# Kernel optimization log

Measured on AMD Instinct MI355X. Metric: run time of the kernel, lower is better.

Reference implementation:

```python
import jax, jax.numpy as jnp
import numpy as np

B, N, K = 32, 64, 128          # batch, atoms per cell, channel width (128x0e + 128x1o)
R_MAX = 5.0
NUM_BESSEL = 8
P_CUT = 5                       # num_polynomial_cutoff
AVG_NEIGH = 16.0                # avg_num_neighbors
H_MLP = 512                     # hidden_dimensions_size, n_hidden_dimensions = 2
FEAT = 5 * K                    # ((num_interactions-1)*4 + 1) * 128 = 640


def silu(x):
    return x * jax.nn.sigmoid(x)


def _bessel_cutoff(r, mask):
    # Bessel radial basis * polynomial cutoff (MACE), masked on valid edges.
    n = jnp.arange(1, NUM_BESSEL + 1, dtype=r.dtype)
    rb = jnp.sqrt(2.0 / R_MAX) * jnp.sin(n * (jnp.pi / R_MAX) * r[..., None]) / r[..., None]
    u = r / R_MAX
    p = float(P_CUT)
    fc = 1.0 - 0.5 * (p + 1) * (p + 2) * u**P_CUT + p * (p + 2) * u**(P_CUT + 1) - 0.5 * p * (p + 1) * u**(P_CUT + 2)
    fc = fc * (u < 1.0)
    return rb * (fc * mask)[..., None]


def _sph(uvec):
    # Real spherical harmonics l=0,1,2 (component normalization), uvec: unit edge vectors.
    x, y, z = uvec[..., 0], uvec[..., 1], uvec[..., 2]
    s3, s5, s15 = 3.0**0.5, 5.0**0.5, 15.0**0.5
    Y0 = jnp.ones_like(x)[..., None]
    Y1 = jnp.stack([s3 * x, s3 * y, s3 * z], -1)
    Y2 = jnp.stack([s15 * x * y, s15 * y * z, 0.5 * s5 * (3 * z * z - 1.0),
                    s15 * x * z, 0.5 * s15 * (x * x - y * y)], -1)
    return Y0, Y1, Y2


def _radial_mlp(x, w0, b0, w1, b1, w2, b2, w3, b3):
    h = silu(x @ w0 + b0)
    h = silu(h @ w1 + b1)
    h = silu(h @ w2 + b2)
    return h @ w3 + b3


def setup_inputs() -> dict:
    key = jax.random.key(0)
    ks = jax.random.split(key, 32)
    f32 = jnp.float32

    def lin(k, fan_in, shape):
        return (jax.random.normal(k, shape, dtype=f32) / np.sqrt(fan_in)).astype(f32)

    inp = {
        "noisy_relative_positions": jax.random.uniform(ks[0], (B, N, 3), dtype=f32),
        "time": jax.random.uniform(ks[1], (B, 1), dtype=f32),
        "unit_cell": (11.0 * jnp.eye(3, dtype=f32) + 0.3 * jax.random.uniform(ks[2], (B, 3, 3), dtype=f32)),
        "w_embed": lin(ks[3], 1, (K,)),
        # interaction 1 radial MLP: 8 -> 64 -> 64 -> 64 -> 3*K (weights for l=0,1,2 paths)
        "r1_w0": lin(ks[4], NUM_BESSEL, (NUM_BESSEL, 64)), "r1_b0": jnp.zeros((64,), f32),
        "r1_w1": lin(ks[5], 64, (64, 64)), "r1_b1": jnp.zeros((64,), f32),
        "r1_w2": lin(ks[6], 64, (64, 64)), "r1_b2": jnp.zeros((64,), f32),
        "r1_w3": lin(ks[7], 64, (64, 3 * K)), "r1_b3": jnp.zeros((3 * K,), f32),
        "mix1_l0": lin(ks[8], K, (K, K)),
        "mix1_l1": lin(ks[9], K, (K, K)),
        "mix1_l2": lin(ks[10], K, (K, K)),
        # interaction 2 radial MLP: 8 -> 64 -> 64 -> 64 -> 2*K (paths 0e x 0e -> 0e, 1o x 1o -> 0e)
        "r2_w0": lin(ks[11], NUM_BESSEL, (NUM_BESSEL, 64)), "r2_b0": jnp.zeros((64,), f32),
        "r2_w1": lin(ks[12], 64, (64, 64)), "r2_b1": jnp.zeros((64,), f32),
        "r2_w2": lin(ks[13], 64, (64, 64)), "r2_b2": jnp.zeros((64,), f32),
        "r2_w3": lin(ks[14], 64, (64, 2 * K)), "r2_b3": jnp.zeros((2 * K,), f32),
        "mix2": lin(ks[15], K, (K, K)),
        # readout MLP: 641 -> 512 -> 512 -> 3
        "mlp_w0": lin(ks[16], FEAT + 1, (FEAT + 1, H_MLP)), "mlp_b0": jnp.zeros((H_MLP,), f32),
        "mlp_w1": lin(ks[17], H_MLP, (H_MLP, H_MLP)), "mlp_b1": jnp.zeros((H_MLP,), f32),
        "mlp_w2": lin(ks[18], H_MLP, (H_MLP, 3)), "mlp_b2": jnp.zeros((3,), f32),
    }
    return inp


def reference(noisy_relative_positions, time, unit_cell, w_embed,
              r1_w0, r1_b0, r1_w1, r1_b1, r1_w2, r1_b2, r1_w3, r1_b3,
              mix1_l0, mix1_l1, mix1_l2,
              r2_w0, r2_b0, r2_w1, r2_b1, r2_w2, r2_b2, r2_w3, r2_b3, mix2,
              mlp_w0, mlp_b0, mlp_w1, mlp_b1, mlp_w2, mlp_b2):
    frac = noisy_relative_positions                      # [B,N,3] fractional
    d = frac[:, :, None, :] - frac[:, None, :, :]        # [B,N,N,3]
    d = d - jnp.round(d)                                 # minimum-image PBC
    dc = jnp.einsum('bijc,bcd->bijd', d, unit_cell)      # cartesian displacements
    r = jnp.sqrt(jnp.maximum(jnp.sum(dc * dc, -1), 1e-12))
    mask = (r < R_MAX) & (~jnp.eye(N, dtype=bool))[None]
    r_safe = jnp.where(mask, r, 1.0)
    uvec = dc / r_safe[..., None] * mask[..., None]      # unit edge vectors (0 off-edge)

    rad = _bessel_cutoff(r_safe, mask)                   # [B,N,N,8]
    Y0, Y1, Y2 = _sph(uvec)                              # [B,N,N,1|3|5]

    h0 = jnp.broadcast_to(w_embed, (B, N, K))            # element embedding (single species)

    # ---- interaction 1: radial-weighted tensor product h_j (x) Y_l, scatter over j ----
    we = _radial_mlp(rad, r1_w0, r1_b0, r1_w1, r1_b1, r1_w2, r1_b2, r1_w3, r1_b3)
    we = we.reshape(B, N, N, 3, K) * mask[..., None, None]
    hj = h0[:, None, :, :]                               # sender features [B,1,N,K]
    msg0 = jnp.einsum('bijk,bijm->bimk', we[..., 0, :] * hj, Y0)[:, :, 0] / AVG_NEIGH  # [B,N,K]
    msg1 = jnp.einsum('bijk,bijm->bimk', we[..., 1, :] * hj, Y1) / AVG_NEIGH           # [B,N,3,K]
    msg2 = jnp.einsum('bijk,bijm->bimk', we[..., 2, :] * hj, Y2) / AVG_NEIGH           # [B,N,5,K]

    s1 = msg0 @ mix1_l0 + jnp.sum(msg2 * msg2, axis=2) @ mix1_l2   # scalars [B,N,K]
    v1 = jnp.einsum('bimk,kc->bimc', msg1, mix1_l1)                # vectors [B,N,3,K]
    h1 = silu(s1)

    # ---- interaction 2: scalar output from 0e x 0e and 1o x 1o -> 0e paths ----
    we2 = _radial_mlp(rad, r2_w0, r2_b0, r2_w1, r2_b1, r2_w2, r2_b2, r2_w3, r2_b3)
    we2 = we2.reshape(B, N, N, 2, K) * mask[..., None, None]
    msg_a = jnp.sum(we2[..., 0, :] * h1[:, None, :, :], axis=2)    # [B,N,K]
    inv = jnp.einsum('bijm,bjmk->bijk', Y1, v1)                    # Y1 . v1_j invariant
    msg_b = jnp.sum(we2[..., 1, :] * inv, axis=2)
    s2 = ((msg_a + msg_b) / AVG_NEIGH) @ mix2                      # [B,N,K]

    # node_feats: layer1 full irreps (128x0e + 128x1o -> 512) + layer2 scalars (128) = 640
    node_feats = jnp.concatenate([s1, v1.reshape(B, N, 3 * K), s2], axis=-1)

    t = jnp.broadcast_to(time[:, None, :], (B, N, 1))
    x = jnp.concatenate([node_feats, t], axis=-1)                  # [B,N,641]
    x = jax.nn.relu(x @ mlp_w0 + mlp_b0)
    x = jax.nn.relu(x @ mlp_w1 + mlp_b1)
    return x @ mlp_w2 + mlp_b2                                     # [B,N,3]
```

## Files before the change

### kernel.cpp

```cpp
#include <hip/hip_runtime.h>
#include <math.h>

#define B_ 32
#define N_ 64
#define K_ 128
#define NPAIR (B_*N_*N_)
#define PREP_TOTAL 733184

typedef __attribute__((ext_vector_type(8))) short short8;
typedef __attribute__((ext_vector_type(8))) __bf16 bf16x8;
typedef __attribute__((ext_vector_type(4))) float floatx4;

__device__ __forceinline__ float silu_f(float x) {
    return x / (1.0f + expf(-x));
}

__device__ __forceinline__ short f2bf(float x) {
    union { float f; unsigned u; } v; v.f = x;
    unsigned r = (v.u + 0x7FFFu + ((v.u >> 16) & 1u)) >> 16;
    return (short)r;
}
__device__ __forceinline__ float bf2f(short s) {
    union { unsigned u; float f; } v;
    v.u = ((unsigned)(unsigned short)s) << 16;
    return v.f;
}
__device__ __forceinline__ bf16x8 ld_frag(const short* p) {
    short8 r = *(const short8*)p;
    return __builtin_bit_cast(bf16x8, r);
}

__global__ __launch_bounds__(256) void prep_kernel(
    const float* __restrict__ r1w1, const float* __restrict__ r1w2,
    const float* __restrict__ r2w1, const float* __restrict__ r2w2,
    const float* __restrict__ r2w3, const float* __restrict__ mw0,
    const float* __restrict__ mw1,
    const float* __restrict__ r1w0, const float* __restrict__ r2w0,
    const float* __restrict__ r1w3,
    const float* __restrict__ l0, const float* __restrict__ l1,
    const float* __restrict__ l2,
    short* __restrict__ dst)
{
    int idx = blockIdx.x * 256 + threadIdx.x;
    if (idx >= PREP_TOTAL) return;
    short v;
    if (idx < 4096) {
        int h = idx >> 6, k = idx & 63; v = f2bf(r1w1[k*64 + h]);
    } else if (idx < 8192) {
        int i = idx - 4096; int h = i >> 6, k = i & 63; v = f2bf(r1w2[k*64 + h]);
    } else if (idx < 12288) {
        int i = idx - 8192; int h = i >> 6, k = i & 63; v = f2bf(r2w1[k*64 + h]);
    } else if (idx < 16384) {
        int i = idx - 12288; int h = i >> 6, k = i & 63; v = f2bf(r2w2[k*64 + h]);
    } else if (idx < 32768) {
        int i = idx - 16384; int col = i >> 6, h = i & 63; v = f2bf(r2w3[h*256 + col]);
    } else if (idx < 393216) {
        int i = idx - 32768; int n = i / 704, k = i - n*704;
        v = (k < 641) ? f2bf(mw0[(size_t)k*512 + n]) : (short)0;
    } else if (idx < 655360) {
        int i = idx - 393216; int n = i >> 9, k = i & 511;
        v = f2bf(mw1[(size_t)k*512 + n]);
    } else if (idx < 657408) {
        int i = idx - 655360; int h = i >> 5, k = i & 31;
        v = (k < 8) ? f2bf(r1w0[k*64 + h]) : (short)0;
    } else if (idx < 659456) {
        int i = idx - 657408; int h = i >> 5, k = i & 31;
        v = (k < 8) ? f2bf(r2w0[k*64 + h]) : (short)0;
    } else if (idx < 684032) {
        int i = idx - 659456; int col = i >> 6, h = i & 63;
        v = f2bf(r1w3[(size_t)h*384 + col]);
    } else {
        int i = idx - 684032; int n = i >> 7, k = i & 127;
        float src = (n < 128) ? l0[(size_t)k*128 + n]
                  : (n < 256) ? l1[(size_t)k*128 + (n-128)]
                              : l2[(size_t)k*128 + (n-256)];
        v = f2bf(src);
    }
    dst[idx] = v;
}

__device__ __forceinline__ void mfma_layer(
    const short* __restrict__ src, const short* __restrict__ WT,
    const float* __restrict__ bias, short* __restrict__ dst,
    int wv, int qd, int nn)
{
    floatx4 acc[4];
    #pragma unroll
    for (int tt = 0; tt < 4; tt++) acc[tt] = (floatx4){0.f, 0.f, 0.f, 0.f};
    #pragma unroll
    for (int ks = 0; ks < 64; ks += 32) {
        bf16x8 a = ld_frag(&src[(wv*16 + nn)*72 + ks + qd*8]);
        #pragma unroll
        for (int tt = 0; tt < 4; tt++) {
            bf16x8 b = ld_frag(&WT[(tt*16 + nn)*64 + ks + qd*8]);
            acc[tt] = __builtin_amdgcn_mfma_f32_16x16x32_bf16(a, b, acc[tt], 0, 0, 0);
        }
    }
    #pragma unroll
    for (int tt = 0; tt < 4; tt++) {
        int col = tt*16 + nn;
        float bv = bias[col];
        #pragma unroll
        for (int i = 0; i < 4; i++) {
            int row = wv*16 + qd*4 + i;
            dst[row*72 + col] = f2bf(silu_f(acc[tt][i] + bv));
        }
    }
}

__device__ __forceinline__ void mfma_layer_T(
    const short* __restrict__ src, const short* __restrict__ WT,
    const float* __restrict__ bias, short* __restrict__ dstT,
    int wv, int qd, int nn)
{
    floatx4 acc[4];
    #pragma unroll
    for (int tt = 0; tt < 4; tt++) acc[tt] = (floatx4){0.f, 0.f, 0.f, 0.f};
    #pragma unroll
    for (int ks = 0; ks < 64; ks += 32) {
        bf16x8 a = ld_frag(&src[(wv*16 + nn)*72 + ks + qd*8]);
        #pragma unroll
        for (int tt = 0; tt < 4; tt++) {
            bf16x8 b = ld_frag(&WT[(tt*16 + nn)*64 + ks + qd*8]);
            acc[tt] = __builtin_amdgcn_mfma_f32_16x16x32_bf16(a, b, acc[tt], 0, 0, 0);
        }
    }
    #pragma unroll
    for (int tt = 0; tt < 4; tt++) {
        int col = tt*16 + nn;
        float bv = bias[col];
        #pragma unroll
        for (int i = 0; i < 4; i++) {
            int row = wv*16 + qd*4 + i;
            dstT[col*72 + row] = f2bf(silu_f(acc[tt][i] + bv));
        }
    }
}

__device__ __forceinline__ void mfma_layer_gout(
    const short* __restrict__ src, const short* __restrict__ WT,
    const float* __restrict__ bias, short* __restrict__ gdst,
    int wv, int qd, int nn)
{
    floatx4 acc[4];
    #pragma unroll
    for (int tt = 0; tt < 4; tt++) acc[tt] = (floatx4){0.f, 0.f, 0.f, 0.f};
    #pragma unroll
    for (int ks = 0; ks < 64; ks += 32) {
        bf16x8 a = ld_frag(&src[(wv*16 + nn)*72 + ks + qd*8]);
        #pragma unroll
        for (int tt = 0; tt < 4; tt++) {
            bf16x8 b = ld_frag(&WT[(tt*16 + nn)*64 + ks + qd*8]);
            acc[tt] = __builtin_amdgcn_mfma_f32_16x16x32_bf16(a, b, acc[tt], 0, 0, 0);
        }
    }
    #pragma unroll
    for (int tt = 0; tt < 4; tt++) {
        int col = tt*16 + nn;
        float bv = bias[col];
        #pragma unroll
        for (int i = 0; i < 4; i++) {
            int row = wv*16 + qd*4 + i;
            gdst[row*64 + col] = f2bf(silu_f(acc[tt][i] + bv));
        }
    }
}

__device__ __forceinline__ void mfma_layer0(
    const short* __restrict__ rad_bf, const short* __restrict__ w0T,
    const float* __restrict__ b0, short* __restrict__ dst,
    int wv, int qd, int nn)
{
    floatx4 acc[4];
    #pragma unroll
    for (int tt = 0; tt < 4; tt++) acc[tt] = (floatx4){0.f, 0.f, 0.f, 0.f};
    bf16x8 a = ld_frag(&rad_bf[(wv*16 + nn)*32 + qd*8]);
    #pragma unroll
    for (int tt = 0; tt < 4; tt++) {
        bf16x8 b = ld_frag(&w0T[(tt*16 + nn)*32 + qd*8]);
        acc[tt] = __builtin_amdgcn_mfma_f32_16x16x32_bf16(a, b, acc[tt], 0, 0, 0);
    }
    #pragma unroll
    for (int tt = 0; tt < 4; tt++) {
        int col = tt*16 + nn;
        float bv = b0[col];
        #pragma unroll
        for (int i = 0; i < 4; i++) {
            int row = wv*16 + qd*4 + i;
            dst[row*72 + col] = f2bf(silu_f(acc[tt][i] + bv));
        }
    }
}

__global__ __launch_bounds__(256) void pass1x_kernel(
    const float* __restrict__ pos, const float* __restrict__ cell,
    const float* __restrict__ wemb,
    const short* __restrict__ w0T1, const float* __restrict__ b01,
    const short* __restrict__ w1T1, const float* __restrict__ b11,
    const short* __restrict__ w2T1, const float* __restrict__ b21,
    const short* __restrict__ w3T1, const float* __restrict__ b31,
    const short* __restrict__ w0T2, const float* __restrict__ b02,
    const short* __restrict__ w1T2, const float* __restrict__ b12,
    const short* __restrict__ w2T2, const float* __restrict__ b22,
    const short* __restrict__ lcatT, const float* __restrict__ timeg,
    float* __restrict__ geo4, short* __restrict__ hc2,
    float* __restrict__ h1g, float* __restrict__ v1g, short* __restrict__ featsb)
{
    __shared__ __align__(16) char smem[41472];
    short* actA   = (short*)smem;
    short* actB   = (short*)(smem + 9216);
    short* actC   = (short*)(smem + 18432);
    short* actD   = (short*)(smem + 27648);
    float* msg    = (float*)(smem + 9216);
    float* q_s    = (float*)(smem + 9216 + 4608);
    short* rad_bf = (short*)(smem + 36864);
    short* Ym_bf  = (short*)(smem + 36864);
    short* G_bf   = (short*)(smem + 36864 + 2304);
    short* A2     = (short*)smem;
    float* Psa    = (float*)(smem + 9216);
    float* Psb    = Psa + 128;

    int t = threadIdx.x;
    int wv = t >> 6, lane = t & 63, qd = lane >> 4, nn = lane & 15;
    int node = blockIdx.x;
    int b = node >> 6;
    int irow = node & 63;
    size_t pbase = (size_t)node * 64;

    float vals[9];
    float sy9[9];
    if (t < 64) {
        int j = t;
        const float* pi = pos + (size_t)(b*N_ + irow)*3;
        const float* pj = pos + (size_t)(b*N_ + j)*3;
        float d0 = pi[0]-pj[0], d1 = pi[1]-pj[1], d2 = pi[2]-pj[2];
        d0 -= rintf(d0); d1 -= rintf(d1); d2 -= rintf(d2);
        const float* C = cell + b*9;
        float dc0 = d0*C[0] + d1*C[3] + d2*C[6];
        float dc1 = d0*C[1] + d1*C[4] + d2*C[7];
        float dc2 = d0*C[2] + d1*C[5] + d2*C[8];
        float r2 = fmaxf(dc0*dc0 + dc1*dc1 + dc2*dc2, 1e-12f);
        float r = sqrtf(r2);
        bool m = (r < 5.0f) && (irow != j);
        float mf = m ? 1.0f : 0.0f;
        float rs = m ? r : 1.0f;
        float inv_rs = 1.0f / rs;
        float x = dc0*inv_rs*mf, y = dc1*inv_rs*mf, z = dc2*inv_rs*mf;
        float u = r * 0.2f;
        float u2 = u*u, u4 = u2*u2, u5 = u4*u;
        float fc = 1.0f - 21.0f*u5 + 35.0f*u5*u - 15.0f*u5*u2;
        fc = (u < 1.0f) ? fc : 0.0f;
        float pref = 0.6324555320336759f * inv_rs * (fc * mf);
        float w = 0.6283185307179586f * rs;
        float sw = sinf(w), cw = cosf(w);
        float twoc = 2.0f * cw;
        float sm = 0.0f, s = sw;
        #pragma unroll
        for (int n = 0; n < 8; n++) {
            rad_bf[j*32 + n] = f2bf(pref * s);
            float nx = twoc*s - sm;
            sm = s; s = nx;
        }
        #pragma unroll
        for (int k = 8; k < 32; k++) rad_bf[j*32 + k] = 0;
        const float s3  = 1.7320508075688772f;
        const float s5  = 2.23606797749979f;
        const float s15 = 3.872983346207417f;
        vals[0] = mf;
        vals[1] = s3*x; vals[2] = s3*y; vals[3] = s3*z;
        vals[4] = s15*x*y;
        vals[5] = s15*y*z;
        vals[6] = 0.5f*s5*(3.0f*z*z - 1.0f);
        vals[7] = s15*x*z;
        vals[8] = 0.5f*s15*(x*x - y*y);
        *(float4*)&geo4[(pbase + j)*4] = make_float4(mf, vals[1], vals[2], vals[3]);
        #pragma unroll
        for (int m9 = 0; m9 < 9; m9++) {
            float sv = vals[m9];
            #pragma unroll
            for (int off = 32; off > 0; off >>= 1) sv += __shfl_xor(sv, off);
            sy9[m9] = sv;
        }
    }
    __syncthreads();

    mfma_layer0(rad_bf, w0T1, b01, actA, wv, qd, nn);
    mfma_layer0(rad_bf, w0T2, b02, actC, wv, qd, nn);
    __syncthreads();

    if (t < 64) {
        int j = t;
        #pragma unroll
        for (int m9 = 0; m9 < 9; m9++) Ym_bf[m9*72 + j] = f2bf(vals[m9]);
        #pragma unroll
        for (int m9 = 9; m9 < 16; m9++) Ym_bf[m9*72 + j] = 0;
        #pragma unroll
        for (int m9 = 0; m9 < 9; m9++)
            if (j == m9) *(float*)(&Ym_bf[m9*72 + 64]) = sy9[m9];
    }
    mfma_layer(actA, w1T1, b11, actB, wv, qd, nn);
    mfma_layer(actC, w1T2, b12, actD, wv, qd, nn);
    __syncthreads();

    mfma_layer_T(actB, w2T1, b21, actA, wv, qd, nn);
    mfma_layer_gout(actD, w2T2, b22, hc2 + (size_t)node*4096, wv, qd, nn);
    __syncthreads();

    {
        floatx4 acc = (floatx4){0.f, 0.f, 0.f, 0.f};
        #pragma unroll
        for (int ks = 0; ks < 64; ks += 32) {
            bf16x8 a = ld_frag(&Ym_bf[nn*72 + ks + qd*8]);
            bf16x8 bb = ld_frag(&actA[(wv*16 + nn)*72 + ks + qd*8]);
            acc = __builtin_amdgcn_mfma_f32_16x16x32_bf16(a, bb, acc, 0, 0, 0);
        }
        #pragma unroll
        for (int i = 0; i < 4; i++)
            G_bf[(qd*4 + i)*72 + wv*16 + nn] = f2bf(acc[i]);
    }
    __syncthreads();

    {
        floatx4 acc[6];
        #pragma unroll
        for (int tt = 0; tt < 6; tt++) acc[tt] = (floatx4){0.f, 0.f, 0.f, 0.f};
        #pragma unroll
        for (int ks = 0; ks < 64; ks += 32) {
            bf16x8 a = ld_frag(&G_bf[nn*72 + ks + qd*8]);
            #pragma unroll
            for (int tt = 0; tt < 6; tt++) {
                bf16x8 bb = ld_frag(&w3T1[((wv*6 + tt)*16 + nn)*64 + ks + qd*8]);
                acc[tt] = __builtin_amdgcn_mfma_f32_16x16x32_bf16(a, bb, acc[tt], 0, 0, 0);
            }
        }
        #pragma unroll
        for (int tt = 0; tt < 6; tt++) {
            int col = (wv*6 + tt)*16 + nn;
            #pragma unroll
            for (int i = 0; i < 4; i++) {
                int m9 = qd*4 + i;
                if (m9 < 9) {
                    int c = (m9 == 0) ? 0 : ((m9 < 4) ? 1 : 2);
                    int k = col - c*128;
                    if (k >= 0 && k < 128) {
                        float sym = *(const float*)(&Ym_bf[m9*72 + 64]);
                        msg[m9*128 + k] = (acc[tt][i] + sym*b31[col]) * wemb[k] * 0.0625f;
                    }
                }
            }
        }
    }
    __syncthreads();

    if (t < 128) {
        int k = t;
        float acc = 0.f;
        #pragma unroll
        for (int m9 = 4; m9 < 9; m9++) { float v = msg[m9*128 + k]; acc += v*v; }
        q_s[k] = acc;
    }
    __syncthreads();

    for (int idx = t; idx < 2048; idx += 256) {
        int r = idx >> 7, k = idx & 127;
        float v = (r == 0) ? msg[k]
                : (r == 1) ? q_s[k]
                : (r < 5)  ? msg[(r-1)*128 + k] : 0.f;
        A2[r*136 + k] = f2bf(v);
    }
    __syncthreads();

    {
        bf16x8 pa[4];
        #pragma unroll
        for (int ksI = 0; ksI < 4; ksI++)
            pa[ksI] = ld_frag(&A2[nn*136 + ksI*32 + qd*8]);
        floatx4 acc[6];
        #pragma unroll
        for (int tt = 0; tt < 6; tt++) acc[tt] = (floatx4){0.f, 0.f, 0.f, 0.f};
        #pragma unroll
        for (int tt = 0; tt < 6; tt++) {
            int tn = wv*6 + tt;
            #pragma unroll
            for (int ksI = 0; ksI < 4; ksI++) {
                bf16x8 bf = ld_frag(&lcatT[((size_t)(tn*16 + nn))*128 + ksI*32 + qd*8]);
                acc[tt] = __builtin_amdgcn_mfma_f32_16x16x32_bf16(pa[ksI], bf, acc[tt], 0, 0, 0);
            }
        }
        #pragma unroll
        for (int tt = 0; tt < 6; tt++) {
            int n = (wv*6 + tt)*16 + nn;
            #pragma unroll
            for (int i = 0; i < 4; i++) {
                int r = qd*4 + i;
                float val = acc[tt][i];
                if (r == 0 && n < 128) Psa[n] = val;
                else if (r == 1 && n >= 256) Psb[n - 256] = val;
                else if (r >= 2 && r < 5 && n >= 128 && n < 256) {
                    int m9 = r - 2, cc = n - 128;
                    v1g[(size_t)node*384 + m9*128 + cc] = val;
                    featsb[(size_t)node*704 + 128 + m9*128 + cc] = f2bf(val);
                }
            }
        }
    }
    __syncthreads();

    if (t < 128) {
        float s1 = Psa[t] + Psb[t];
        featsb[(size_t)node*704 + t] = f2bf(s1);
        h1g[(size_t)node*128 + t] = silu_f(s1);
    } else if (t == 128) {
        featsb[(size_t)node*704 + 640] = f2bf(timeg[b]);
    } else if (t > 128 && t < 192) {
        featsb[(size_t)node*704 + 640 + (t - 128)] = 0;
    }
}

__global__ __launch_bounds__(256) void pass2b_kernel(
    const float* __restrict__ geo4,
    const short* __restrict__ hc2,
    const short* __restrict__ w3T, const float* __restrict__ b3,
    const float* __restrict__ mix2,
    const float* __restrict__ h1g, const float* __restrict__ v1g,
    short* __restrict__ featsb)
{
    __shared__ float mask_s[64];
    __shared__ float Y1s[64*4];
    __shared__ float msgab[128];
    int t = threadIdx.x;
    int wv = t >> 6, lane = t & 63, qd = lane >> 4, nn = lane & 15;
    int node = blockIdx.x;
    int b = node >> 6;
    size_t pbase = (size_t)node * 64;

    if (t < 64) {
        float4 g = *(const float4*)&geo4[(pbase + t)*4];
        mask_s[t] = g.x;
        Y1s[t*4 + 0] = g.y; Y1s[t*4 + 1] = g.z; Y1s[t*4 + 2] = g.w;
    }
    if (t >= 64 && t < 192) msgab[t - 64] = 0.f;
    __syncthreads();

    const short* hcb = hc2 + (size_t)node*4096;
    bf16x8 a0 = ld_frag(&hcb[(wv*16 + nn)*64 + qd*8]);
    bf16x8 a1 = ld_frag(&hcb[(wv*16 + nn)*64 + 32 + qd*8]);
    for (int g = 0; g < 4; g++) {
        floatx4 acc[4];
        #pragma unroll
        for (int tt = 0; tt < 4; tt++) acc[tt] = (floatx4){0.f, 0.f, 0.f, 0.f};
        #pragma unroll
        for (int tt = 0; tt < 4; tt++) {
            int ct = g*4 + tt;
            bf16x8 b0f = ld_frag(&w3T[(ct*16 + nn)*64 + qd*8]);
            bf16x8 b1f = ld_frag(&w3T[(ct*16 + nn)*64 + 32 + qd*8]);
            acc[tt] = __builtin_amdgcn_mfma_f32_16x16x32_bf16(a0, b0f, acc[tt], 0, 0, 0);
            acc[tt] = __builtin_amdgcn_mfma_f32_16x16x32_bf16(a1, b1f, acc[tt], 0, 0, 0);
        }
        #pragma unroll
        for (int tt = 0; tt < 4; tt++) {
            int col = (g*4 + tt)*16 + nn;
            float bias = b3[col];
            int k = col & 127;
            float p = 0.f;
            if (col < 128) {
                #pragma unroll
                for (int i = 0; i < 4; i++) {
                    int j = wv*16 + qd*4 + i;
                    float we = (acc[tt][i] + bias) * mask_s[j];
                    p += we * h1g[((size_t)b*64 + j)*128 + k];
                }
            } else {
                #pragma unroll
                for (int i = 0; i < 4; i++) {
                    int j = wv*16 + qd*4 + i;
                    float we = (acc[tt][i] + bias) * mask_s[j];
                    const float* vb = &v1g[((size_t)b*64 + j)*384 + k];
                    float inv = Y1s[j*4+0]*vb[0] + Y1s[j*4+1]*vb[128] + Y1s[j*4+2]*vb[256];
                    p += we * inv;
                }
            }
            p += __shfl_xor(p, 16);
            p += __shfl_xor(p, 32);
            if (qd == 0) atomicAdd(&msgab[k], p);
        }
    }
    __syncthreads();

    if (t < 128) {
        int c = t;
        float acc = 0.f;
        for (int k = 0; k < 128; k++) acc += msgab[k] * mix2[k*128 + c];
        featsb[(size_t)node*704 + 512 + c] = f2bf(acc * 0.0625f);
    }
}

__global__ __launch_bounds__(256) void gemm_mfma_kernel(
    const short* __restrict__ A, int lda,
    const short* __restrict__ BT, int ldb, int K,
    const float* __restrict__ bias, short* __restrict__ Cout, int ldo)
{
    __shared__ short As[64*72];
    __shared__ short Bs[64*72];
    int t = threadIdx.x;
    int wv = t >> 6, lane = t & 63, qd = lane >> 4, nn = lane & 15;
    int m0 = blockIdx.x * 64, n0 = blockIdx.y * 64;
    floatx4 acc[4];
    #pragma unroll
    for (int tt = 0; tt < 4; tt++) acc[tt] = (floatx4){0.f, 0.f, 0.f, 0.f};

    for (int kc = 0; kc < K; kc += 64) {
        for (int s = t; s < 512; s += 256) {
            int j = s >> 3, kk = (s & 7) * 8;
            *(uint4*)&As[j*72 + kk] = *(const uint4*)&A[(size_t)(m0 + j)*lda + kc + kk];
            *(uint4*)&Bs[j*72 + kk] = *(const uint4*)&BT[(size_t)(n0 + j)*ldb + kc + kk];
        }
        __syncthreads();
        #pragma unroll
        for (int ks = 0; ks < 64; ks += 32) {
            bf16x8 a = ld_frag(&As[(wv*16 + nn)*72 + ks + qd*8]);
            #pragma unroll
            for (int tt = 0; tt < 4; tt++) {
                bf16x8 bb = ld_frag(&Bs[(tt*16 + nn)*72 + ks + qd*8]);
                acc[tt] = __builtin_amdgcn_mfma_f32_16x16x32_bf16(a, bb, acc[tt], 0, 0, 0);
            }
        }
        __syncthreads();
    }
    #pragma unroll
    for (int tt = 0; tt < 4; tt++) {
        int n = n0 + tt*16 + nn;
        float bv = bias[n];
        #pragma unroll
        for (int i = 0; i < 4; i++) {
            int m = m0 + wv*16 + qd*4 + i;
            Cout[(size_t)m*ldo + n] = f2bf(fmaxf(acc[tt][i] + bv, 0.f));
        }
    }
}

__global__ __launch_bounds__(64) void final3_kernel(
    const short* __restrict__ H, const float* __restrict__ w2,
    const float* __restrict__ b2, float* __restrict__ out)
{
    int node = blockIdx.x, lane = threadIdx.x;
    float a0 = 0.f, a1 = 0.f, a2 = 0.f;
    #pragma unroll
    for (int r = 0; r < 8; r++) {
        int k = r*64 + lane;
        float h = bf2f(H[(size_t)node*512 + k]);
        a0 += h * w2[k*3 + 0];
        a1 += h * w2[k*3 + 1];
        a2 += h * w2[k*3 + 2];
    }
    #pragma unroll
    for (int off = 32; off > 0; off >>= 1) {
        a0 += __shfl_down(a0, off);
        a1 += __shfl_down(a1, off);
        a2 += __shfl_down(a2, off);
    }
    if (lane == 0) {
        out[(size_t)node*3 + 0] = a0 + b2[0];
        out[(size_t)node*3 + 1] = a1 + b2[1];
        out[(size_t)node*3 + 2] = a2 + b2[2];
    }
}

extern "C" void kernel_launch(void* const* d_in, const int* in_sizes, int n_in,
                              void* d_out, int out_size, void* d_ws, size_t ws_size,
                              hipStream_t stream) {
    const float* pos   = (const float*)d_in[0];
    const float* timeg = (const float*)d_in[1];
    const float* cell  = (const float*)d_in[2];
    const float* wemb  = (const float*)d_in[3];
    const float* r1w0  = (const float*)d_in[4];
    const float* r1b0  = (const float*)d_in[5];
    const float* r1w1  = (const float*)d_in[6];
    const float* r1b1  = (const float*)d_in[7];
    const float* r1w2  = (const float*)d_in[8];
    const float* r1b2  = (const float*)d_in[9];
    const float* r1w3  = (const float*)d_in[10];
    const float* r1b3  = (const float*)d_in[11];
    const float* l0    = (const float*)d_in[12];
    const float* l1    = (const float*)d_in[13];
    const float* l2    = (const float*)d_in[14];
    const float* r2w0  = (const float*)d_in[15];
    const float* r2b0  = (const float*)d_in[16];
    const float* r2w1  = (const float*)d_in[17];
    const float* r2b1  = (const float*)d_in[18];
    const float* r2w2  = (const float*)d_in[19];
    const float* r2b2  = (const float*)d_in[20];
    const float* r2w3  = (const float*)d_in[21];
    const float* r2b3  = (const float*)d_in[22];
    const float* mix2  = (const float*)d_in[23];
    const float* mw0   = (const float*)d_in[24];
    const float* mb0   = (const float*)d_in[25];
    const float* mw1   = (const float*)d_in[26];
    const float* mb1   = (const float*)d_in[27];
    const float* mw2   = (const float*)d_in[28];
    const float* mb2   = (const float*)d_in[29];

    float* ws    = (float*)d_ws;
    float* geo4  = ws;
    float* h1    = geo4 + (size_t)NPAIR*4;
    float* v1    = h1   + (size_t)B_*N_*K_;
    short* featsb = (short*)(v1 + (size_t)B_*N_*3*K_);
    short* prep  = featsb + (size_t)2048*704;
    short* w1T_1 = prep;
    short* w2T_1 = prep + 4096;
    short* w1T_2 = prep + 8192;
    short* w2T_2 = prep + 12288;
    short* w3T_2 = prep + 16384;
    short* wT0   = prep + 32768;
    short* wT1   = prep + 393216;
    short* w0T_1 = prep + 655360;
    short* w0T_2 = prep + 657408;
    short* w3T_1 = prep + 659456;
    short* lcatT = prep + 684032;
    short* hc2   = prep + PREP_TOTAL;
    short* h0bb  = hc2 + (size_t)2048*4096;
    short* h1bb  = h0bb + (size_t)2048*512;

    prep_kernel<<<(PREP_TOTAL + 255)/256, 256, 0, stream>>>(
        r1w1, r1w2, r2w1, r2w2, r2w3, mw0, mw1,
        r1w0, r2w0, r1w3, l0, l1, l2, prep);
    pass1x_kernel<<<B_*N_, 256, 0, stream>>>(pos, cell, wemb,
        w0T_1, r1b0, w1T_1, r1b1, w2T_1, r1b2, w3T_1, r1b3,
        w0T_2, r2b0, w1T_2, r2b1, w2T_2, r2b2,
        lcatT, timeg, geo4, hc2, h1, v1, featsb);
    pass2b_kernel<<<B_*N_, 256, 0, stream>>>(geo4, hc2,
        w3T_2, r2b3, mix2, h1, v1, featsb);
    dim3 g0(32, 8);
    gemm_mfma_kernel<<<g0, 256, 0, stream>>>(featsb, 704, wT0, 704, 704, mb0, h0bb, 512);
    gemm_mfma_kernel<<<g0, 256, 0, stream>>>(h0bb, 512, wT1, 512, 512, mb1, h1bb, 512);
    final3_kernel<<<B_*N_, 64, 0, stream>>>(h1bb, mw2, mb2, (float*)d_out);
}
```

Measured before the change: 288.5 us.

## Split pass1 into MLP kernel and back-projection kernel to cut LDS footprint

```diff
diff --git a/kernel.cpp b/kernel.cpp
--- a/kernel.cpp
+++ b/kernel.cpp
@@ -12,7 +12,7 @@
 typedef __attribute__((ext_vector_type(4))) float floatx4;
 
 __device__ __forceinline__ float silu_f(float x) {
-    return x / (1.0f + expf(-x));
+    return x / (1.0f + __expf(-x));
 }
 
 __device__ __forceinline__ short f2bf(float x) {
@@ -192,34 +192,20 @@
     }
 }
 
-__global__ __launch_bounds__(256) void pass1x_kernel(
+__global__ __launch_bounds__(256) void mlpx_kernel(
     const float* __restrict__ pos, const float* __restrict__ cell,
-    const float* __restrict__ wemb,
     const short* __restrict__ w0T1, const float* __restrict__ b01,
     const short* __restrict__ w1T1, const float* __restrict__ b11,
     const short* __restrict__ w2T1, const float* __restrict__ b21,
-    const short* __restrict__ w3T1, const float* __restrict__ b31,
     const short* __restrict__ w0T2, const float* __restrict__ b02,
     const short* __restrict__ w1T2, const float* __restrict__ b12,
     const short* __restrict__ w2T2, const float* __restrict__ b22,
-    const short* __restrict__ lcatT, const float* __restrict__ timeg,
-    float* __restrict__ geo4, short* __restrict__ hc2,
-    float* __restrict__ h1g, float* __restrict__ v1g, short* __restrict__ featsb)
-{
-    __shared__ __align__(16) char smem[41472];
-    short* actA   = (short*)smem;
-    short* actB   = (short*)(smem + 9216);
-    short* actC   = (short*)(smem + 18432);
-    short* actD   = (short*)(smem + 27648);
-    float* msg    = (float*)(smem + 9216);
-    float* q_s    = (float*)(smem + 9216 + 4608);
-    short* rad_bf = (short*)(smem + 36864);
-    short* Ym_bf  = (short*)(smem + 36864);
-    short* G_bf   = (short*)(smem + 36864 + 2304);
-    short* A2     = (short*)smem;
-    float* Psa    = (float*)(smem + 9216);
-    float* Psb    = Psa + 128;
-
+    float* __restrict__ geo4, short* __restrict__ hc2, short* __restrict__ Gg)
+{
+    __shared__ __align__(16) short actA[64*72];
+    __shared__ __align__(16) short actB[64*72];
+    __shared__ __align__(16) short rad_bf[64*32];
+    __shared__ __align__(16) short Ym_bf[16*72];
     int t = threadIdx.x;
     int wv = t >> 6, lane = t & 63, qd = lane >> 4, nn = lane & 15;
     int node = blockIdx.x;
@@ -227,8 +213,6 @@
     int irow = node & 63;
     size_t pbase = (size_t)node * 64;
 
-    float vals[9];
-    float sy9[9];
     if (t < 64) {
         int j = t;
         const float* pi = pos + (size_t)(b*N_ + irow)*3;
@@ -266,6 +250,7 @@
         const float s3  = 1.7320508075688772f;
         const float s5  = 2.23606797749979f;
         const float s15 = 3.872983346207417f;
+        float vals[9];
         vals[0] = mf;
         vals[1] = s3*x; vals[2] = s3*y; vals[3] = s3*z;
         vals[4] = s15*x*y;
@@ -275,35 +260,34 @@
         vals[8] = 0.5f*s15*(x*x - y*y);
         *(float4*)&geo4[(pbase + j)*4] = make_float4(mf, vals[1], vals[2], vals[3]);
         #pragma unroll
+        for (int m9 = 0; m9 < 9; m9++) Ym_bf[m9*72 + j] = f2bf(vals[m9]);
+        #pragma unroll
+        for (int m9 = 9; m9 < 16; m9++) Ym_bf[m9*72 + j] = 0;
+        #pragma unroll
         for (int m9 = 0; m9 < 9; m9++) {
             float sv = vals[m9];
             #pragma unroll
             for (int off = 32; off > 0; off >>= 1) sv += __shfl_xor(sv, off);
-            sy9[m9] = sv;
-        }
-    }
-    __syncthreads();
-
+            if (j == m9)
+                *(float*)(Gg + (size_t)node*1152 + m9*72 + 64) = sv;
+        }
+    }
+    __syncthreads();
+
+    mfma_layer0(rad_bf, w0T2, b02, actA, wv, qd, nn);
+    __syncthreads();
+
+    mfma_layer(actA, w1T2, b12, actB, wv, qd, nn);
+    __syncthreads();
+
+    mfma_layer_gout(actB, w2T2, b22, hc2 + (size_t)node*4096, wv, qd, nn);
     mfma_layer0(rad_bf, w0T1, b01, actA, wv, qd, nn);
-    mfma_layer0(rad_bf, w0T2, b02, actC, wv, qd, nn);
-    __syncthreads();
-
-    if (t < 64) {
-        int j = t;
-        #pragma unroll
-        for (int m9 = 0; m9 < 9; m9++) Ym_bf[m9*72 + j] = f2bf(vals[m9]);
-        #pragma unroll
-        for (int m9 = 9; m9 < 16; m9++) Ym_bf[m9*72 + j] = 0;
-        #pragma unroll
-        for (int m9 = 0; m9 < 9; m9++)
-            if (j == m9) *(float*)(&Ym_bf[m9*72 + 64]) = sy9[m9];
-    }
+    __syncthreads();
+
     mfma_layer(actA, w1T1, b11, actB, wv, qd, nn);
-    mfma_layer(actC, w1T2, b12, actD, wv, qd, nn);
     __syncthreads();
 
     mfma_layer_T(actB, w2T1, b21, actA, wv, qd, nn);
-    mfma_layer_gout(actD, w2T2, b22, hc2 + (size_t)node*4096, wv, qd, nn);
     __syncthreads();
 
     {
@@ -316,22 +300,45 @@
         }
         #pragma unroll
         for (int i = 0; i < 4; i++)
-            G_bf[(qd*4 + i)*72 + wv*16 + nn] = f2bf(acc[i]);
-    }
+            Gg[(size_t)node*1152 + (qd*4 + i)*72 + wv*16 + nn] = f2bf(acc[i]);
+    }
+}
+
+__global__ __launch_bounds__(256) void back1_kernel(
+    const float* __restrict__ wemb,
+    const short* __restrict__ Gg,
+    const short* __restrict__ w3T, const float* __restrict__ b3,
+    const short* __restrict__ lcatT, const float* __restrict__ timeg,
+    float* __restrict__ h1g, float* __restrict__ v1g, short* __restrict__ featsb)
+{
+    __shared__ __align__(16) short G_lds[16*72];
+    __shared__ __align__(16) short A2[16*136];
+    __shared__ float q_s[128];
+    __shared__ float Ps[256];
+    int t = threadIdx.x;
+    int wv = t >> 6, lane = t & 63, qd = lane >> 4, nn = lane & 15;
+    int node = blockIdx.x;
+    int b = node >> 6;
+
+    if (t < 144)
+        ((uint4*)G_lds)[t] = ((const uint4*)(Gg + (size_t)node*1152))[t];
+    if (t < 128) q_s[t] = 0.f;
+    for (int z = 680 + t; z < 2176; z += 256) A2[z] = 0;
     __syncthreads();
 
     {
+        bf16x8 ga0 = ld_frag(&G_lds[nn*72 + qd*8]);
+        bf16x8 ga1 = ld_frag(&G_lds[nn*72 + 32 + qd*8]);
         floatx4 acc[6];
         #pragma unroll
         for (int tt = 0; tt < 6; tt++) acc[tt] = (floatx4){0.f, 0.f, 0.f, 0.f};
         #pragma unroll
-        for (int ks = 0; ks < 64; ks += 32) {
-            bf16x8 a = ld_frag(&G_bf[nn*72 + ks + qd*8]);
-            #pragma unroll
-            for (int tt = 0; tt < 6; tt++) {
-                bf16x8 bb = ld_frag(&w3T1[((wv*6 + tt)*16 + nn)*64 + ks + qd*8]);
-                acc[tt] = __builtin_amdgcn_mfma_f32_16x16x32_bf16(a, bb, acc[tt], 0, 0, 0);
-            }
+        for (int tt = 0; tt < 6; tt++) {
+            int tn = wv*6 + tt;
+            bf16x8 b0f = ld_frag(&w3T[(tn*16 + nn)*64 + qd*8]);
+            bf16x8 b1f = ld_frag(&w3T[(tn*16 + nn)*64 + 32 + qd*8]);
+            acc[tt] = __builtin_amdgcn_mfma_f32_16x16x32_bf16(ga0, b0f, acc[tt], 0, 0, 0);
+            acc[tt] = __builtin_amdgcn_mfma_f32_16x16x32_bf16(ga1, b1f, acc[tt], 0, 0, 0);
         }
         #pragma unroll
         for (int tt = 0; tt < 6; tt++) {
@@ -343,8 +350,11 @@
                     int c = (m9 == 0) ? 0 : ((m9 < 4) ? 1 : 2);
                     int k = col - c*128;
                     if (k >= 0 && k < 128) {
-                        float sym = *(const float*)(&Ym_bf[m9*72 + 64]);
-                        msg[m9*128 + k] = (acc[tt][i] + sym*b31[col]) * wemb[k] * 0.0625f;
+                        float sym = *(const float*)(&G_lds[m9*72 + 64]);
+                        float val = (acc[tt][i] + sym*b3[col]) * wemb[k] * 0.0625f;
+                        if (m9 == 0)      A2[k] = f2bf(val);
+                        else if (m9 < 4)  A2[(m9+1)*136 + k] = f2bf(val);
+                        else              atomicAdd(&q_s[k], val*val);
                     }
                 }
             }
@@ -352,22 +362,7 @@
     }
     __syncthreads();
 
-    if (t < 128) {
-        int k = t;
-        float acc = 0.f;
-        #pragma unroll
-        for (int m9 = 4; m9 < 9; m9++) { float v = msg[m9*128 + k]; acc += v*v; }
-        q_s[k] = acc;
-    }
-    __syncthreads();
-
-    for (int idx = t; idx < 2048; idx += 256) {
-        int r = idx >> 7, k = idx & 127;
-        float v = (r == 0) ? msg[k]
-                : (r == 1) ? q_s[k]
-                : (r < 5)  ? msg[(r-1)*128 + k] : 0.f;
-        A2[r*136 + k] = f2bf(v);
-    }
+    if (t < 128) A2[136 + t] = f2bf(q_s[t]);
     __syncthreads();
 
     {
@@ -394,8 +389,8 @@
             for (int i = 0; i < 4; i++) {
                 int r = qd*4 + i;
                 float val = acc[tt][i];
-                if (r == 0 && n < 128) Psa[n] = val;
-                else if (r == 1 && n >= 256) Psb[n - 256] = val;
+                if (r == 0 && n < 128) Ps[n] = val;
+                else if (r == 1 && n >= 256) Ps[128 + n - 256] = val;
                 else if (r >= 2 && r < 5 && n >= 128 && n < 256) {
                     int m9 = r - 2, cc = n - 128;
                     v1g[(size_t)node*384 + m9*128 + cc] = val;
@@ -407,7 +402,7 @@
     __syncthreads();
 
     if (t < 128) {
-        float s1 = Psa[t] + Psb[t];
+        float s1 = Ps[t] + Ps[128 + t];
         featsb[(size_t)node*704 + t] = f2bf(s1);
         h1g[(size_t)node*128 + t] = silu_f(s1);
     } else if (t == 128) {
@@ -618,16 +613,19 @@
     short* w3T_1 = prep + 659456;
     short* lcatT = prep + 684032;
     short* hc2   = prep + PREP_TOTAL;
-    short* h0bb  = hc2 + (size_t)2048*4096;
-    short* h1bb  = h0bb + (size_t)2048*512;
+    short* Gg    = hc2 + (size_t)2048*4096;
+    short* h0bb  = hc2;
+    short* h1bb  = hc2 + (size_t)2048*512;
 
     prep_kernel<<<(PREP_TOTAL + 255)/256, 256, 0, stream>>>(
         r1w1, r1w2, r2w1, r2w2, r2w3, mw0, mw1,
         r1w0, r2w0, r1w3, l0, l1, l2, prep);
-    pass1x_kernel<<<B_*N_, 256, 0, stream>>>(pos, cell, wemb,
-        w0T_1, r1b0, w1T_1, r1b1, w2T_1, r1b2, w3T_1, r1b3,
+    mlpx_kernel<<<B_*N_, 256, 0, stream>>>(pos, cell,
+        w0T_1, r1b0, w1T_1, r1b1, w2T_1, r1b2,
         w0T_2, r2b0, w1T_2, r2b1, w2T_2, r2b2,
-        lcatT, timeg, geo4, hc2, h1, v1, featsb);
+        geo4, hc2, Gg);
+    back1_kernel<<<B_*N_, 256, 0, stream>>>(wemb, Gg,
+        w3T_1, r1b3, lcatT, timeg, h1, v1, featsb);
     pass2b_kernel<<<B_*N_, 256, 0, stream>>>(geo4, hc2,
         w3T_2, r2b3, mix2, h1, v1, featsb);
     dim3 g0(32, 8);
```

New measurement: 289.1 us. About the same (+0.2%).
